# Performance work log

Measured on AMD Instinct MI355X. Metric: run time of the kernel, lower is better.

The kernel has to match this reference:

```python
import jax, jax.numpy as jnp
import numpy as np

N = 30000          # nodes
E = 480000         # edges (before self-loops)
G = 64             # graphs in batch
EMB = 64
IN = 6 + 2 * EMB   # 134
H1, C1 = 4, 128    # gat1 heads / out channels
H2, C2 = 1, 256    # gat2
LRELU_SLOPE = 0.2


def _layernorm(x, g, b, eps=1e-5):
    m = x.mean(-1, keepdims=True)
    v = ((x - m) ** 2).mean(-1, keepdims=True)
    return (x - m) / jnp.sqrt(v + eps) * g + b


def _gatv2(x, src, dst, Wl, bl, Wr, br, att, bias, H, C, n, concat):
    # GATv2 (PyG semantics, share_weights=False, eval mode -> no dropout)
    xl = (x @ Wl + bl).reshape(n, H, C)   # source transform
    xr = (x @ Wr + br).reshape(n, H, C)   # target transform
    # e_ij = att . leaky_relu(xl_j + xr_i), edges j->i : [E_tot, H]
    e = jnp.sum(jax.nn.leaky_relu(xl[src] + xr[dst], LRELU_SLOPE) * att, axis=-1)
    # scatter-softmax over incoming edges of each target node
    emax = jax.lax.stop_gradient(jax.ops.segment_max(e, dst, num_segments=n))
    ex = jnp.exp(e - emax[dst])
    den = jax.ops.segment_sum(ex, dst, num_segments=n)
    alpha = ex / (den[dst] + 1e-16)                       # [E_tot, H]
    out = jax.ops.segment_sum(alpha[:, :, None] * xl[src], dst, num_segments=n)
    if concat:
        return out.reshape(n, H * C) + bias
    return out.mean(axis=1) + bias


def setup_inputs() -> dict:
    key = jax.random.key(0)
    ks = jax.random.split(key, 24)
    s = 0.05
    inp = {
        "x_cont": jax.random.normal(ks[0], (N, 6), jnp.float32),
        "x_class": jax.random.randint(ks[1], (N,), 0, 12, jnp.int32),
        "x_pitch": jax.random.randint(ks[2], (N,), 0, 129, jnp.int32),
        "edge_index": jax.random.randint(ks[3], (2, E), 0, N, jnp.int32),
        "batch": jnp.sort(jax.random.randint(ks[4], (N,), 0, G, jnp.int32)),
        "class_tab": jax.random.normal(ks[5], (12, EMB), jnp.float32) * s,
        "pitch_tab": jax.random.normal(ks[6], (129, EMB), jnp.float32) * s,
        "Wl1": jax.random.normal(ks[7], (IN, H1 * C1), jnp.float32) * s,
        "bl1": jnp.zeros((H1 * C1,), jnp.float32),
        "Wr1": jax.random.normal(ks[8], (IN, H1 * C1), jnp.float32) * s,
        "br1": jnp.zeros((H1 * C1,), jnp.float32),
        "att1": jax.random.normal(ks[9], (H1, C1), jnp.float32) * s,
        "bias1": jnp.zeros((H1 * C1,), jnp.float32),
        "ln1_g": jnp.ones((H1 * C1,), jnp.float32),
        "ln1_b": jnp.zeros((H1 * C1,), jnp.float32),
        "Wl2": jax.random.normal(ks[10], (H1 * C1, H2 * C2), jnp.float32) * s,
        "bl2": jnp.zeros((H2 * C2,), jnp.float32),
        "Wr2": jax.random.normal(ks[11], (H1 * C1, H2 * C2), jnp.float32) * s,
        "br2": jnp.zeros((H2 * C2,), jnp.float32),
        "att2": jax.random.normal(ks[12], (H2, C2), jnp.float32) * s,
        "bias2": jnp.zeros((C2,), jnp.float32),
        "ln2_g": jnp.ones((C2,), jnp.float32),
        "ln2_b": jnp.zeros((C2,), jnp.float32),
        "Wp1": jax.random.normal(ks[13], (C2, 512), jnp.float32) * s,
        "bp1": jnp.zeros((512,), jnp.float32),
        "lnp_g": jnp.ones((512,), jnp.float32),
        "lnp_b": jnp.zeros((512,), jnp.float32),
        "Wp2": jax.random.normal(ks[14], (512, 512), jnp.float32) * s,
        "bp2": jnp.zeros((512,), jnp.float32),
    }
    return inp


def reference(x_cont, x_class, x_pitch, edge_index, batch,
              class_tab, pitch_tab,
              Wl1, bl1, Wr1, br1, att1, bias1, ln1_g, ln1_b,
              Wl2, bl2, Wr2, br2, att2, bias2, ln2_g, ln2_b,
              Wp1, bp1, lnp_g, lnp_b, Wp2, bp2):
    # node features: [N, 6 + 64 + 64]
    x = jnp.concatenate([x_cont, class_tab[x_class], pitch_tab[x_pitch]], axis=1)
    # add self-loops (PyG GATv2Conv default)
    loops = jnp.arange(N, dtype=edge_index.dtype)
    src = jnp.concatenate([edge_index[0], loops])
    dst = jnp.concatenate([edge_index[1], loops])
    x = jax.nn.elu(_layernorm(_gatv2(x, src, dst, Wl1, bl1, Wr1, br1, att1, bias1, H1, C1, N, True), ln1_g, ln1_b))
    x = jax.nn.elu(_layernorm(_gatv2(x, src, dst, Wl2, bl2, Wr2, br2, att2, bias2, H2, C2, N, False), ln2_g, ln2_b))
    # global mean pool over graphs
    sums = jax.ops.segment_sum(x, batch, num_segments=G)
    cnt = jax.ops.segment_sum(jnp.ones((N,), x.dtype), batch, num_segments=G)
    pooled = sums / jnp.maximum(cnt, 1.0)[:, None]
    # projection head + L2 normalize
    h = jax.nn.gelu(_layernorm(pooled @ Wp1 + bp1, lnp_g, lnp_b), approximate=False)
    out = h @ Wp2 + bp2
    norm = jnp.sqrt(jnp.sum(out * out, axis=1, keepdims=True))
    return out / jnp.maximum(norm, 1e-12)
```

## Files before the change

kernel.cpp:

```cpp
#include <hip/hip_runtime.h>
#include <math.h>

#define NG 64

typedef short bf16x8 __attribute__((ext_vector_type(8)));
typedef short bf16x4 __attribute__((ext_vector_type(4)));
typedef float f32x4 __attribute__((ext_vector_type(4)));

#define LOG2E 1.4426950408889634f

static inline int cdiv(int a, int b) { return (a + b - 1) / b; }

__device__ inline ushort f2b(float f) {
  union { float f; uint u; } v; v.f = f;
  uint u = v.u;
  return (ushort)((u + 0x7fffu + ((u >> 16) & 1u)) >> 16);
}

__device__ __forceinline__ void unpack8(bf16x8 vb, float* v) {
  union { bf16x8 b; uint u[4]; } cv; cv.b = vb;
#pragma unroll
  for (int q = 0; q < 4; ++q) {
    union { uint u; float f; } lo, hi;
    lo.u = cv.u[q] << 16;
    hi.u = cv.u[q] & 0xffff0000u;
    v[2 * q] = lo.f; v[2 * q + 1] = hi.f;
  }
}
__device__ __forceinline__ void unpack4(bf16x4 vb, float* v) {
  union { bf16x4 b; uint u[2]; } cv; cv.b = vb;
#pragma unroll
  for (int q = 0; q < 2; ++q) {
    union { uint u; float f; } lo, hi;
    lo.u = cv.u[q] << 16;
    hi.u = cv.u[q] & 0xffff0000u;
    v[2 * q] = lo.f; v[2 * q + 1] = hi.f;
  }
}

__device__ __forceinline__ float dppsum16(float x) {
  union { float f; int i; } a, b;
  a.f = x;
  b.i = __builtin_amdgcn_update_dpp(0, a.i, 0x121, 0xF, 0xF, true); a.f += b.f;
  b.i = __builtin_amdgcn_update_dpp(0, a.i, 0x122, 0xF, 0xF, true); a.f += b.f;
  b.i = __builtin_amdgcn_update_dpp(0, a.i, 0x124, 0xF, 0xF, true); a.f += b.f;
  b.i = __builtin_amdgcn_update_dpp(0, a.i, 0x128, 0xF, 0xF, true); a.f += b.f;
  return a.f;
}

// ... 89 lines not shown
}

__global__ __launch_bounds__(256) void k_scatter(
    const int* __restrict__ src, const int* __restrict__ dst,
    const int* __restrict__ rowptr, int* __restrict__ fill,
    int* __restrict__ csr, int E, int N) {
  int t = blockIdx.x * blockDim.x + threadIdx.x;
  int s, d;
  if (t < E) { s = src[t]; d = dst[t]; }
  else if (t < E + N) { s = t - E; d = t - E; }
  else if (t < E + N + 8) { csr[t] = 0; return; }
  else return;
  int pos = rowptr[d] + atomicAdd(&fill[d], 1);
  csr[pos] = s;
}

#define GBM 128
#define GBN 128
#define GBK 32
#define ESTRIDE 136
__device__ __forceinline__ int swzf(int r, int s) {
  return r * 64 + ((s * 16) ^ (((r >> 1) & 3) << 4));
}
__global__ __launch_bounds__(256) void k_gemm_mfma(
    const ushort* __restrict__ A, const ushort* __restrict__ Bt,
    const float* __restrict__ blo, const float* __restrict__ bhi, int nhalf,
    ushort* __restrict__ Clo, ushort* __restrict__ Chi, int M, int Kp) {
  __shared__ ushort smem[GBM * ESTRIDE];
  ushort* sA = smem;
  ushort* sB = smem + GBM * GBK;
  int tid = threadIdx.x;
  int lane = tid & 63, w = tid >> 6;
  int wr = w >> 1, wc = w & 1;
  int row0 = blockIdx.x * GBM, col0 = blockIdx.y * GBN;
  int nK = Kp / GBK;

  int rs = tid >> 2, ss = tid & 3;
  int wO0 = swzf(rs, ss);
  int wO1 = swzf(rs + 64, ss);
  bool okA0 = (row0 + rs) < M;
  bool okA1 = (row0 + rs + 64) < M;
  size_t baseA0 = (size_t)(row0 + rs) * Kp + ss * 8;
  size_t baseA1 = (size_t)(row0 + rs + 64) * Kp + ss * 8;
  size_t baseB0 = (size_t)(col0 + rs) * Kp + ss * 8;
  size_t baseB1 = (size_t)(col0 + rs + 64) * Kp + ss * 8;

  int fr = lane & 15, kq = lane >> 4;
  int aoff[4], boff[4];
#pragma unroll
  for (int m = 0; m < 4; ++m) {
    int ra = wr * 64 + m * 16 + fr;
    aoff[m] = ra * 64 + ((kq * 16) ^ (((ra >> 1) & 3) << 4));
    int rb = wc * 64 + m * 16 + fr;
    boff[m] = rb * 64 + ((kq * 16) ^ (((rb >> 1) & 3) << 4));
  }

  f32x4 acc[4][4] = {};
  bf16x8 zz = {};
  bf16x8 pa0, pa1, pb0, pb1, qa0, qa1, qb0, qb1;

#define LOADG(KS, RA0, RA1, RB0, RB1)                                   \
  do {                                                                  \
    const ushort* ap = A + (size_t)(KS) * GBK;                          \
    const ushort* bp = Bt + (size_t)(KS) * GBK;                         \
    RA0 = okA0 ? *(const bf16x8*)(ap + baseA0) : zz;                    \
    RA1 = okA1 ? *(const bf16x8*)(ap + baseA1) : zz;                    \
    RB0 = *(const bf16x8*)(bp + baseB0);                                \
// ... 37 lines not shown

  __syncthreads();
#pragma unroll
  for (int m = 0; m < 4; ++m) {
#pragma unroll
    for (int n = 0; n < 4; ++n) {
      int tc = wc * 64 + n * 16 + fr;
      float bv = ((col0 + tc) < nhalf) ? blo[col0 + tc] : bhi[col0 + tc - nhalf];
#pragma unroll
      for (int j = 0; j < 4; ++j) {
        int tr = wr * 64 + m * 16 + kq * 4 + j;
        smem[tr * ESTRIDE + tc] = f2b(acc[m][n][j] + bv);
      }
    }
  }
  __syncthreads();
  ushort* Cd = (col0 < nhalf) ? Clo : Chi;
  int cb0 = (col0 < nhalf) ? col0 : col0 - nhalf;
  int r0 = tid >> 4, cb = (tid & 15) * 8;
#pragma unroll
  for (int pass = 0; pass < 8; ++pass) {
    int r = pass * 16 + r0;
    int grow = row0 + r;
    if (grow < M) {
      bf16x8 vv = *(const bf16x8*)&smem[r * ESTRIDE + cb];
      *(bf16x8*)&Cd[(size_t)grow * nhalf + cb0 + cb] = vv;
    }
  }
#undef LOADG
#undef STAGE
#undef COMPUTE
}

__global__ __launch_bounds__(256, 4) void k_gat1(
    const ushort* __restrict__ xl, const ushort* __restrict__ xr,
    const int* __restrict__ rowptr, const int* __restrict__ csr,
    const float* __restrict__ att, const float* __restrict__ bias,
    const float* __restrict__ lng, const float* __restrict__ lnb,
    ushort* __restrict__ out, int n) {
  int lane = threadIdx.x & 63;
  int wid = __builtin_amdgcn_readfirstlane((int)((blockIdx.x * blockDim.x + threadIdx.x) >> 6));
  if (wid >= n) return;
  int base = lane * 8;
  float xrv[8], a6[8], a4[8];
  {
    bf16x8 t = *(const bf16x8*)(xr + (size_t)wid * 512 + base);
    unpack8(t, xrv);
#pragma unroll
    for (int j = 0; j < 8; ++j) {
      float a = att[base + j] * LOG2E;
      a6[j] = 0.6f * a;
      a4[j] = 0.4f * a;
    }
  }
  float s = 0.f;
  float acc[8] = {};
  int e0 = rowptr[wid], e1 = rowptr[wid + 1];
  int last = e1 - 1;

#define LROW1(ROW) (*(const bf16x8*)(xl + (size_t)(ROW) * 512 + base))
  bf16x8 r0 = LROW1(csr[e0]);
  bf16x8 r1 = LROW1(csr[min(e0 + 1, last)]);
  bf16x8 r2 = LROW1(csr[min(e0 + 2, last)]);
  bf16x8 r3 = LROW1(csr[min(e0 + 3, last)]);

  for (int pp = e0; pp < e1; pp += 4) {
    int i0 = csr[min(pp + 4, last)], i1 = csr[min(pp + 5, last)];
    int i2 = csr[min(pp + 6, last)], i3 = csr[min(pp + 7, last)];
    bf16x8 c0 = r0, c1 = r1, c2 = r2, c3 = r3;
    r0 = LROW1(i0); r1 = LROW1(i1); r2 = LROW1(i2); r3 = LROW1(i3);
    float v0[8], v1[8], v2[8], v3[8];
    unpack8(c0, v0); unpack8(c1, v1); unpack8(c2, v2); unpack8(c3, v3);
    float p0 = 0.f, p1 = 0.f, p2 = 0.f, p3 = 0.f;
#pragma unroll
    for (int j = 0; j < 8; ++j) {
      float t0 = v0[j] + xrv[j];
      float t1 = v1[j] + xrv[j];
      float t2 = v2[j] + xrv[j];
      float t3 = v3[j] + xrv[j];
      p0 = fmaf(a6[j], t0, fmaf(a4[j], fabsf(t0), p0));
      p1 = fmaf(a6[j], t1, fmaf(a4[j], fabsf(t1), p1));
      p2 = fmaf(a6[j], t2, fmaf(a4[j], fabsf(t2), p2));
      p3 = fmaf(a6[j], t3, fmaf(a4[j], fabsf(t3), p3));
    }
    float pe0 = dppsum16(p0);
    float pe1 = dppsum16(p1);
    float pe2 = dppsum16(p2);
    float pe3 = dppsum16(p3);
    float w0 = exp2f(pe0 - 8.f * LOG2E);
    float w1 = (pp + 1 <= last) ? exp2f(pe1 - 8.f * LOG2E) : 0.f;
    float w2 = (pp + 2 <= last) ? exp2f(pe2 - 8.f * LOG2E) : 0.f;
    float w3 = (pp + 3 <= last) ? exp2f(pe3 - 8.f * LOG2E) : 0.f;
    s += (w0 + w1) + (w2 + w3);
#pragma unroll
    for (int j = 0; j < 8; ++j) {
      float t = fmaf(w0, v0[j], acc[j]);
      t = fmaf(w1, v1[j], t);
      t = fmaf(w2, v2[j], t);
      acc[j] = fmaf(w3, v3[j], t);
    }
  }
#undef LROW1
  float inv = 1.f / s;
  float o[8];
#pragma unroll
  for (int j = 0; j < 8; ++j) o[j] = acc[j] * inv + bias[base + j];
  float sum = 0.f, sq = 0.f;
#pragma unroll
  for (int j = 0; j < 8; ++j) { sum += o[j]; sq += o[j] * o[j]; }
  sum = dppsum16(sum); sq = dppsum16(sq);
  sum += __shfl_xor(sum, 16); sq += __shfl_xor(sq, 16);
  sum += __shfl_xor(sum, 32); sq += __shfl_xor(sq, 32);
  float mean = sum * (1.f / 512.f);
  float var = fmaxf(sq * (1.f / 512.f) - mean * mean, 0.f);
  float rstd = rsqrtf(var + 1e-5f);
  bf16x8 ov;
#pragma unroll
  for (int j = 0; j < 8; ++j) {
    float y = (o[j] - mean) * rstd * lng[base + j] + lnb[base + j];
    y = y > 0.f ? y : __expf(y) - 1.f;
    ov[j] = (short)f2b(y);
  }
  *(bf16x8*)&out[(size_t)wid * 512 + base] = ov;
}

__global__ __launch_bounds__(256, 4) void k_gat2(
    const ushort* __restrict__ xl, const ushort* __restrict__ xr,
    const int* __restrict__ rowptr, const int* __restrict__ csr,
    const float* __restrict__ att, const float* __restrict__ bias,
    const float* __restrict__ lng, const float* __restrict__ lnb,
    float* __restrict__ out, int n) {
  int lane = threadIdx.x & 63;
  int wid = __builtin_amdgcn_readfirstlane((int)((blockIdx.x * blockDim.x + threadIdx.x) >> 6));
  if (wid >= n) return;
  int base = lane * 4;
  float xrv[4], a6[4], a4[4];
  {
    bf16x4 t = *(const bf16x4*)(xr + (size_t)wid * 256 + base);
    unpack4(t, xrv);
#pragma unroll
    for (int j = 0; j < 4; ++j) {
      float a = att[base + j] * LOG2E;
      a6[j] = 0.6f * a;
      a4[j] = 0.4f * a;
    }
  }
  float s = 0.f;
  float acc[4] = {};
  int e0 = rowptr[wid], e1 = rowptr[wid + 1];
  int last = e1 - 1;

#define LROW2(ROW) (*(const bf16x4*)(xl + (size_t)(ROW) * 256 + base))
  bf16x4 r0 = LROW2(csr[e0]);
  bf16x4 r1 = LROW2(csr[min(e0 + 1, last)]);
  bf16x4 r2 = LROW2(csr[min(e0 + 2, last)]);
  bf16x4 r3 = LROW2(csr[min(e0 + 3, last)]);

  for (int pp = e0; pp < e1; pp += 4) {
    int i0 = csr[min(pp + 4, last)], i1 = csr[min(pp + 5, last)];
    int i2 = csr[min(pp + 6, last)], i3 = csr[min(pp + 7, last)];
    bf16x4 c0 = r0, c1 = r1, c2 = r2, c3 = r3;
    r0 = LROW2(i0); r1 = LROW2(i1); r2 = LROW2(i2); r3 = LROW2(i3);
    float v0[4], v1[4], v2[4], v3[4];
    unpack4(c0, v0); unpack4(c1, v1); unpack4(c2, v2); unpack4(c3, v3);
    float p0 = 0.f, p1 = 0.f, p2 = 0.f, p3 = 0.f;
#pragma unroll
    for (int j = 0; j < 4; ++j) {
      float t0 = v0[j] + xrv[j];
      float t1 = v1[j] + xrv[j];
      float t2 = v2[j] + xrv[j];
      float t3 = v3[j] + xrv[j];
      p0 = fmaf(a6[j], t0, fmaf(a4[j], fabsf(t0), p0));
      p1 = fmaf(a6[j], t1, fmaf(a4[j], fabsf(t1), p1));
      p2 = fmaf(a6[j], t2, fmaf(a4[j], fabsf(t2), p2));
      p3 = fmaf(a6[j], t3, fmaf(a4[j], fabsf(t3), p3));
    }
    float pe0 = dppsum16(p0);
    float pe1 = dppsum16(p1);
    float pe2 = dppsum16(p2);
    float pe3 = dppsum16(p3);
    pe0 += __shfl_xor(pe0, 16); pe1 += __shfl_xor(pe1, 16);
    pe2 += __shfl_xor(pe2, 16); pe3 += __shfl_xor(pe3, 16);
    pe0 += __shfl_xor(pe0, 32); pe1 += __shfl_xor(pe1, 32);
    pe2 += __shfl_xor(pe2, 32); pe3 += __shfl_xor(pe3, 32);
    float w0 = exp2f(pe0 - 8.f * LOG2E);
    float w1 = (pp + 1 <= last) ? exp2f(pe1 - 8.f * LOG2E) : 0.f;
    float w2 = (pp + 2 <= last) ? exp2f(pe2 - 8.f * LOG2E) : 0.f;
    float w3 = (pp + 3 <= last) ? exp2f(pe3 - 8.f * LOG2E) : 0.f;
    s += (w0 + w1) + (w2 + w3);
#pragma unroll
    for (int j = 0; j < 4; ++j) {
      float t = fmaf(w0, v0[j], acc[j]);
      t = fmaf(w1, v1[j], t);
      t = fmaf(w2, v2[j], t);
      acc[j] = fmaf(w3, v3[j], t);
    }
  }
#undef LROW2
  float inv = 1.f / s;
  float o[4];
#pragma unroll
  for (int j = 0; j < 4; ++j) o[j] = acc[j] * inv + bias[base + j];
  float sum = 0.f, sq = 0.f;
#pragma unroll
  for (int j = 0; j < 4; ++j) { sum += o[j]; sq += o[j] * o[j]; }
  sum = dppsum16(sum); sq = dppsum16(sq);
  sum += __shfl_xor(sum, 16); sq += __shfl_xor(sq, 16);
  sum += __shfl_xor(sum, 32); sq += __shfl_xor(sq, 32);
  float mean = sum * (1.f / 256.f);
  float var = fmaxf(sq * (1.f / 256.f) - mean * mean, 0.f);
  float rstd = rsqrtf(var + 1e-5f);
#pragma unroll
  for (int j = 0; j < 4; ++j) {
    float y = (o[j] - mean) * rstd * lng[base + j] + lnb[base + j];
    y = y > 0.f ? y : __expf(y) - 1.f;
    out[(size_t)wid * 256 + base + j] = y;
  }
}

__global__ __launch_bounds__(256) void k_pool(
    const float* __restrict__ h2, const int* __restrict__ batch,
    float* __restrict__ pooled, int* __restrict__ cnt, int n) {
  int c = threadIdx.x;
  int n0 = blockIdx.x * 64;
  int n1 = min(n0 + 64, n);
  if (n0 >= n) return;
  float acc = 0.f;
  int cur = batch[n0];
  int cl = 0;
  for (int i = n0; i < n1; ++i) {
    int bb = batch[i];
    if (bb != cur) {
      atomicAdd(&pooled[cur * 256 + c], acc);
      if (c == 0) atomicAdd(&cnt[cur], cl);
      acc = 0.f; cl = 0; cur = bb;
    }
    acc += h2[(size_t)i * 256 + c];
    cl++;
  }
  atomicAdd(&pooled[cur * 256 + c], acc);
  if (c == 0) atomicAdd(&cnt[cur], cl);
}

__global__ __launch_bounds__(512) void k_proj1(
    const float* __restrict__ pooled, const int* __restrict__ cnt,
    const float* __restrict__ W, const float* __restrict__ b,
    const float* __restrict__ lng, const float* __restrict__ lnb,
    float* __restrict__ hout) {
  __shared__ float row[256];
  __shared__ float red[16];
  int g = blockIdx.x, c = threadIdx.x;
  if (c < 256) {
    float cc = fmaxf((float)cnt[g], 1.f);
    row[c] = pooled[g * 256 + c] / cc;
  }
  __syncthreads();
  float acc = b[c];
#pragma unroll 4
  for (int k = 0; k < 256; ++k) acc += row[k] * W[k * 512 + c];
  float sum = acc, sq = acc * acc;
#pragma unroll
  for (int off = 1; off < 64; off <<= 1) {
    sum += __shfl_xor(sum, off);
    sq += __shfl_xor(sq, off);
  }
  int wv = threadIdx.x >> 6;
  if ((threadIdx.x & 63) == 0) { red[wv] = sum; red[8 + wv] = sq; }
  __syncthreads();
  float S = 0.f, Q = 0.f;
#pragma unroll
// ... 58 lines not shown
  const float* ln2b = (const float*)d_in[22];
  const float* Wp1 = (const float*)d_in[23];
  const float* bp1 = (const float*)d_in[24];
  const float* lnpg = (const float*)d_in[25];
  const float* lnpb = (const float*)d_in[26];
  const float* Wp2 = (const float*)d_in[27];
  const float* bp2 = (const float*)d_in[28];
  float* out = (float*)d_out;
  (void)n_in; (void)out_size; (void)ws_size;

  int N = in_sizes[1];
  int E = in_sizes[3] / 2;
  int ET = E + N;
  int NB = cdiv(N, 256);

  char* p = (char*)d_ws;
  ushort* xb   = (ushort*)p; p += (size_t)N * 160 * 2;
  ushort* W1t  = (ushort*)p; p += (size_t)1024 * 160 * 2;
  ushort* W2t  = (ushort*)p; p += (size_t)512 * 512 * 2;
  ushort* xl1  = (ushort*)p; p += (size_t)N * 512 * 2;
  ushort* xr1  = (ushort*)p; p += (size_t)N * 512 * 2;
  ushort* h1b  = (ushort*)p; p += (size_t)N * 512 * 2;
  float* pooled = (float*)p; p += (size_t)NG * 256 * 4;
  int* cnt     = (int*)p;    p += NG * 4;
  float* hproj = (float*)p;  p += (size_t)NG * 512 * 4;
  int* deg     = (int*)p;    p += (size_t)N * 4;
  int* fill    = (int*)p;    p += (size_t)N * 4;
  int* rowptr  = (int*)p;    p += (size_t)(N + 1) * 4;
  int* csr     = (int*)p;    p += (size_t)(ET + 8) * 4;
  int* bsum    = (int*)p;    p += 256 * 4;
  int* boff    = (int*)p;    p += 256 * 4;
  ushort* xl2 = xl1;
  ushort* xr2 = xl1 + (size_t)N * 256;
  float* h2   = (float*)xr1;

  const int* esrc = ei;
  const int* edst = ei + E;

  hipMemsetAsync(deg, 0, (size_t)2 * N * sizeof(int), stream);
  hipMemsetAsync(pooled, 0, (size_t)NG * 256 * sizeof(float) + NG * sizeof(int), stream);

  int prep_total = N * 160 + 1024 * 160 + 512 * 512 + ET;
  k_prep<<<cdiv(prep_total, 256), 256, 0, stream>>>(
      x_cont, x_class, x_pitch, ctab, ptab, Wl1, Wr1, Wl2, Wr2, edst,
      xb, W1t, W2t, deg, N, E);
  k_bsum<<<NB, 256, 0, stream>>>(deg, bsum, N);
  k_scanb<<<1, 256, 0, stream>>>(bsum, boff, NB);
  k_scanc<<<NB, 256, 0, stream>>>(deg, boff, rowptr, N);
  k_scatter<<<cdiv(ET + 8, 256), 256, 0, stream>>>(esrc, edst, rowptr, fill, csr, E, N);

  dim3 g1(cdiv(N, GBM), 1024 / GBN);
  k_gemm_mfma<<<g1, 256, 0, stream>>>(xb, W1t, bl1, br1, 512, xl1, xr1, N, 160);
  k_gat1<<<cdiv(N * 64, 256), 256, 0, stream>>>(xl1, xr1, rowptr, csr, att1, bias1, ln1g, ln1b, h1b, N);

  dim3 g2(cdiv(N, GBM), 512 / GBN);
  k_gemm_mfma<<<g2, 256, 0, stream>>>(h1b, W2t, bl2, br2, 256, xl2, xr2, N, 512);
  k_gat2<<<cdiv(N * 64, 256), 256, 0, stream>>>(xl2, xr2, rowptr, csr, att2, bias2, ln2g, ln2b, h2, N);

  k_pool<<<cdiv(N, 64), 256, 0, stream>>>(h2, batch, pooled, cnt, N);
  k_proj1<<<NG, 512, 0, stream>>>(pooled, cnt, Wp1, bp1, lnpg, lnpb, hproj);
  k_proj2<<<NG, 512, 0, stream>>>(hproj, Wp2, bp2, out);
}
```

Baseline: 333.7 us.

## Enlarge GAT blocks, split score accumulators, store layer-2 output as bf16

Both GAT aggregation kernels now launch 1024-thread blocks with launch bounds (1024, 8), which pushes for more resident waves to hide gather latency at the cost of register pressure. The attention-score dot products use two interleaved accumulators per edge to shorten FMA dependency chains. The layer-2 output is written as bf16 instead of fp32 and converted back in the pooling kernel, halving that write and read traffic while adding rounding error before pooling.

After: 497.2 us. +49.0%, slower.

```diff
diff --git a/kernel.cpp b/kernel.cpp
--- a/kernel.cpp
+++ b/kernel.cpp
@@ -15,6 +15,10 @@
   union { float f; uint u; } v; v.f = f;
   uint u = v.u;
   return (ushort)((u + 0x7fffu + ((u >> 16) & 1u)) >> 16);
+}
+__device__ inline float b2f(ushort h) {
+  union { uint u; float f; } v; v.u = ((uint)h) << 16;
+  return v.f;
 }
 
 __device__ __forceinline__ void unpack8(bf16x8 vb, float* v) {
@@ -274,7 +278,7 @@
 #undef COMPUTE
 }
 
-__global__ __launch_bounds__(256, 4) void k_gat1(
+__global__ __launch_bounds__(1024, 8) void k_gat1(
     const ushort* __restrict__ xl, const ushort* __restrict__ xr,
     const int* __restrict__ rowptr, const int* __restrict__ csr,
     const float* __restrict__ att, const float* __restrict__ bias,
@@ -313,22 +317,28 @@
     r0 = LROW1(i0); r1 = LROW1(i1); r2 = LROW1(i2); r3 = LROW1(i3);
     float v0[8], v1[8], v2[8], v3[8];
     unpack8(c0, v0); unpack8(c1, v1); unpack8(c2, v2); unpack8(c3, v3);
-    float p0 = 0.f, p1 = 0.f, p2 = 0.f, p3 = 0.f;
-#pragma unroll
-    for (int j = 0; j < 8; ++j) {
-      float t0 = v0[j] + xrv[j];
-      float t1 = v1[j] + xrv[j];
-      float t2 = v2[j] + xrv[j];
-      float t3 = v3[j] + xrv[j];
-      p0 = fmaf(a6[j], t0, fmaf(a4[j], fabsf(t0), p0));
-      p1 = fmaf(a6[j], t1, fmaf(a4[j], fabsf(t1), p1));
-      p2 = fmaf(a6[j], t2, fmaf(a4[j], fabsf(t2), p2));
-      p3 = fmaf(a6[j], t3, fmaf(a4[j], fabsf(t3), p3));
-    }
-    float pe0 = dppsum16(p0);
-    float pe1 = dppsum16(p1);
-    float pe2 = dppsum16(p2);
-    float pe3 = dppsum16(p3);
+    float p0a = 0.f, p0b = 0.f, p1a = 0.f, p1b = 0.f;
+    float p2a = 0.f, p2b = 0.f, p3a = 0.f, p3b = 0.f;
+#pragma unroll
+    for (int q = 0; q < 4; ++q) {
+      int ja = 2 * q, jb = 2 * q + 1;
+      float t0a = v0[ja] + xrv[ja], t0b = v0[jb] + xrv[jb];
+      float t1a = v1[ja] + xrv[ja], t1b = v1[jb] + xrv[jb];
+      float t2a = v2[ja] + xrv[ja], t2b = v2[jb] + xrv[jb];
+      float t3a = v3[ja] + xrv[ja], t3b = v3[jb] + xrv[jb];
+      p0a = fmaf(a6[ja], t0a, fmaf(a4[ja], fabsf(t0a), p0a));
+      p0b = fmaf(a6[jb], t0b, fmaf(a4[jb], fabsf(t0b), p0b));
+      p1a = fmaf(a6[ja], t1a, fmaf(a4[ja], fabsf(t1a), p1a));
+      p1b = fmaf(a6[jb], t1b, fmaf(a4[jb], fabsf(t1b), p1b));
+      p2a = fmaf(a6[ja], t2a, fmaf(a4[ja], fabsf(t2a), p2a));
+      p2b = fmaf(a6[jb], t2b, fmaf(a4[jb], fabsf(t2b), p2b));
+      p3a = fmaf(a6[ja], t3a, fmaf(a4[ja], fabsf(t3a), p3a));
+      p3b = fmaf(a6[jb], t3b, fmaf(a4[jb], fabsf(t3b), p3b));
+    }
+    float pe0 = dppsum16(p0a + p0b);
+    float pe1 = dppsum16(p1a + p1b);
+    float pe2 = dppsum16(p2a + p2b);
+    float pe3 = dppsum16(p3a + p3b);
     float w0 = exp2f(pe0 - 8.f * LOG2E);
     float w1 = (pp + 1 <= last) ? exp2f(pe1 - 8.f * LOG2E) : 0.f;
     float w2 = (pp + 2 <= last) ? exp2f(pe2 - 8.f * LOG2E) : 0.f;
@@ -366,12 +376,12 @@
   *(bf16x8*)&out[(size_t)wid * 512 + base] = ov;
 }
 
-__global__ __launch_bounds__(256, 4) void k_gat2(
+__global__ __launch_bounds__(1024, 8) void k_gat2(
     const ushort* __restrict__ xl, const ushort* __restrict__ xr,
     const int* __restrict__ rowptr, const int* __restrict__ csr,
     const float* __restrict__ att, const float* __restrict__ bias,
     const float* __restrict__ lng, const float* __restrict__ lnb,
-    float* __restrict__ out, int n) {
+    ushort* __restrict__ out, int n) {
   int lane = threadIdx.x & 63;
   int wid = __builtin_amdgcn_readfirstlane((int)((blockIdx.x * blockDim.x + threadIdx.x) >> 6));
   if (wid >= n) return;
@@ -405,22 +415,28 @@
     r0 = LROW2(i0); r1 = LROW2(i1); r2 = LROW2(i2); r3 = LROW2(i3);
     float v0[4], v1[4], v2[4], v3[4];
     unpack4(c0, v0); unpack4(c1, v1); unpack4(c2, v2); unpack4(c3, v3);
-    float p0 = 0.f, p1 = 0.f, p2 = 0.f, p3 = 0.f;
-#pragma unroll
-    for (int j = 0; j < 4; ++j) {
-      float t0 = v0[j] + xrv[j];
-      float t1 = v1[j] + xrv[j];
-      float t2 = v2[j] + xrv[j];
-      float t3 = v3[j] + xrv[j];
-      p0 = fmaf(a6[j], t0, fmaf(a4[j], fabsf(t0), p0));
-      p1 = fmaf(a6[j], t1, fmaf(a4[j], fabsf(t1), p1));
-      p2 = fmaf(a6[j], t2, fmaf(a4[j], fabsf(t2), p2));
-      p3 = fmaf(a6[j], t3, fmaf(a4[j], fabsf(t3), p3));
-    }
-    float pe0 = dppsum16(p0);
-    float pe1 = dppsum16(p1);
-    float pe2 = dppsum16(p2);
-    float pe3 = dppsum16(p3);
+    float p0a = 0.f, p0b = 0.f, p1a = 0.f, p1b = 0.f;
+    float p2a = 0.f, p2b = 0.f, p3a = 0.f, p3b = 0.f;
+#pragma unroll
+    for (int q = 0; q < 2; ++q) {
+      int ja = 2 * q, jb = 2 * q + 1;
+      float t0a = v0[ja] + xrv[ja], t0b = v0[jb] + xrv[jb];
+      float t1a = v1[ja] + xrv[ja], t1b = v1[jb] + xrv[jb];
+      float t2a = v2[ja] + xrv[ja], t2b = v2[jb] + xrv[jb];
+      float t3a = v3[ja] + xrv[ja], t3b = v3[jb] + xrv[jb];
+      p0a = fmaf(a6[ja], t0a, fmaf(a4[ja], fabsf(t0a), p0a));
+      p0b = fmaf(a6[jb], t0b, fmaf(a4[jb], fabsf(t0b), p0b));
+      p1a = fmaf(a6[ja], t1a, fmaf(a4[ja], fabsf(t1a), p1a));
+      p1b = fmaf(a6[jb], t1b, fmaf(a4[jb], fabsf(t1b), p1b));
+      p2a = fmaf(a6[ja], t2a, fmaf(a4[ja], fabsf(t2a), p2a));
+      p2b = fmaf(a6[jb], t2b, fmaf(a4[jb], fabsf(t2b), p2b));
+      p3a = fmaf(a6[ja], t3a, fmaf(a4[ja], fabsf(t3a), p3a));
+      p3b = fmaf(a6[jb], t3b, fmaf(a4[jb], fabsf(t3b), p3b));
+    }
+    float pe0 = dppsum16(p0a + p0b);
+    float pe1 = dppsum16(p1a + p1b);
+    float pe2 = dppsum16(p2a + p2b);
+    float pe3 = dppsum16(p3a + p3b);
     pe0 += __shfl_xor(pe0, 16); pe1 += __shfl_xor(pe1, 16);
     pe2 += __shfl_xor(pe2, 16); pe3 += __shfl_xor(pe3, 16);
     pe0 += __shfl_xor(pe0, 32); pe1 += __shfl_xor(pe1, 32);
@@ -452,16 +468,18 @@
   float mean = sum * (1.f / 256.f);
   float var = fmaxf(sq * (1.f / 256.f) - mean * mean, 0.f);
   float rstd = rsqrtf(var + 1e-5f);
+  bf16x4 ov;
 #pragma unroll
   for (int j = 0; j < 4; ++j) {
     float y = (o[j] - mean) * rstd * lng[base + j] + lnb[base + j];
     y = y > 0.f ? y : __expf(y) - 1.f;
-    out[(size_t)wid * 256 + base + j] = y;
-  }
+    ov[j] = (short)f2b(y);
+  }
+  *(bf16x4*)&out[(size_t)wid * 256 + base] = ov;
 }
 
 __global__ __launch_bounds__(256) void k_pool(
-    const float* __restrict__ h2, const int* __restrict__ batch,
+    const ushort* __restrict__ h2, const int* __restrict__ batch,
     float* __restrict__ pooled, int* __restrict__ cnt, int n) {
   int c = threadIdx.x;
   int n0 = blockIdx.x * 64;
@@ -477,7 +495,7 @@
       if (c == 0) atomicAdd(&cnt[cur], cl);
       acc = 0.f; cl = 0; cur = bb;
     }
-    acc += h2[(size_t)i * 256 + c];
+    acc += b2f(h2[(size_t)i * 256 + c]);
     cl++;
   }
   atomicAdd(&pooled[cur * 256 + c], acc);
@@ -602,7 +620,7 @@
   int* boff    = (int*)p;    p += 256 * 4;
   ushort* xl2 = xl1;
   ushort* xr2 = xl1 + (size_t)N * 256;
-  float* h2   = (float*)xr1;
+  ushort* h2  = xr1;
 
   const int* esrc = ei;
   const int* edst = ei + E;
@@ -621,11 +639,11 @@
 
   dim3 g1(cdiv(N, GBM), 1024 / GBN);
   k_gemm_mfma<<<g1, 256, 0, stream>>>(xb, W1t, bl1, br1, 512, xl1, xr1, N, 160);
-  k_gat1<<<cdiv(N * 64, 256), 256, 0, stream>>>(xl1, xr1, rowptr, csr, att1, bias1, ln1g, ln1b, h1b, N);
+  k_gat1<<<cdiv(N * 64, 1024), 1024, 0, stream>>>(xl1, xr1, rowptr, csr, att1, bias1, ln1g, ln1b, h1b, N);
 
   dim3 g2(cdiv(N, GBM), 512 / GBN);
   k_gemm_mfma<<<g2, 256, 0, stream>>>(h1b, W2t, bl2, br2, 256, xl2, xr2, N, 512);
-  k_gat2<<<cdiv(N * 64, 256), 256, 0, stream>>>(xl2, xr2, rowptr, csr, att2, bias2, ln2g, ln2b, h2, N);
+  k_gat2<<<cdiv(N * 64, 1024), 1024, 0, stream>>>(xl2, xr2, rowptr, csr, att2, bias2, ln2g, ln2b, h2, N);
 
   k_pool<<<cdiv(N, 64), 256, 0, stream>>>(h2, batch, pooled, cnt, N);
   k_proj1<<<NG, 512, 0, stream>>>(pooled, cnt, Wp1, bp1, lnpg, lnpb, hproj);
```

## Process two nodes per wavefront in GAT kernels, bf16 h2, swap GEMM grid order

Applied to the files above, without the earlier changes.

Each wavefront in the GAT aggregation kernels now handles two target nodes at once and interleaves their neighbor gathers, so more independent loads are in flight. The dot-product reduction is split into two partial sums to shorten the dependency chain. The layer-2 output is stored as bf16 instead of fp32, which halves the bytes the pool kernel reads, at some precision cost. The GEMM grid swaps its x/y axes so column tiles of the same row block run next to each other for better A-tile cache reuse. Pairing nodes of different degrees wastes work up to the larger degree and adds register pressure (launch bounds lowered to 3).

Result: slower. 351.0 us (+5.2%).

```diff
diff --git a/kernel.cpp b/kernel.cpp
--- a/kernel.cpp
+++ b/kernel.cpp
@@ -15,6 +15,10 @@
   union { float f; uint u; } v; v.f = f;
   uint u = v.u;
   return (ushort)((u + 0x7fffu + ((u >> 16) & 1u)) >> 16);
+}
+__device__ inline float b2f(ushort h) {
+  union { uint u; float f; } v; v.u = ((uint)h) << 16;
+  return v.f;
 }
 
 __device__ __forceinline__ void unpack8(bf16x8 vb, float* v) {
@@ -170,7 +174,7 @@
   int tid = threadIdx.x;
   int lane = tid & 63, w = tid >> 6;
   int wr = w >> 1, wc = w & 1;
-  int row0 = blockIdx.x * GBM, col0 = blockIdx.y * GBN;
+  int row0 = blockIdx.y * GBM, col0 = blockIdx.x * GBN;
   int nK = Kp / GBK;
 
   int rs = tid >> 2, ss = tid & 3;
@@ -274,194 +278,262 @@
 #undef COMPUTE
 }
 
-__global__ __launch_bounds__(256, 4) void k_gat1(
+__global__ __launch_bounds__(256, 3) void k_gat1(
     const ushort* __restrict__ xl, const ushort* __restrict__ xr,
     const int* __restrict__ rowptr, const int* __restrict__ csr,
     const float* __restrict__ att, const float* __restrict__ bias,
     const float* __restrict__ lng, const float* __restrict__ lnb,
     ushort* __restrict__ out, int n) {
   int lane = threadIdx.x & 63;
-  int wid = __builtin_amdgcn_readfirstlane((int)((blockIdx.x * blockDim.x + threadIdx.x) >> 6));
-  if (wid >= n) return;
+  int wp = __builtin_amdgcn_readfirstlane((int)((blockIdx.x * blockDim.x + threadIdx.x) >> 6));
+  int widA = wp * 2;
+  if (widA >= n) return;
+  bool hasB = (widA + 1) < n;
+  int widB = hasB ? widA + 1 : widA;
   int base = lane * 8;
-  float xrv[8], a6[8], a4[8];
-  {
-    bf16x8 t = *(const bf16x8*)(xr + (size_t)wid * 512 + base);
-    unpack8(t, xrv);
-#pragma unroll
-    for (int j = 0; j < 8; ++j) {
-      float a = att[base + j] * LOG2E;
-      a6[j] = 0.6f * a;
-      a4[j] = 0.4f * a;
-    }
-  }
-  float s = 0.f;
-  float acc[8] = {};
-  int e0 = rowptr[wid], e1 = rowptr[wid + 1];
-  int last = e1 - 1;
+  float a6[8], a4[8];
+#pragma unroll
+  for (int j = 0; j < 8; ++j) {
+    float a = att[base + j] * LOG2E;
+    a6[j] = 0.6f * a;
+    a4[j] = 0.4f * a;
+  }
+  float xrA[8], xrB[8];
+  unpack8(*(const bf16x8*)(xr + (size_t)widA * 512 + base), xrA);
+  unpack8(*(const bf16x8*)(xr + (size_t)widB * 512 + base), xrB);
+  float sA = 0.f, sB = 0.f;
+  float accA[8] = {}, accB[8] = {};
+  int eA0 = rowptr[widA], dA = rowptr[widA + 1] - eA0, lastA = eA0 + dA - 1;
+  int eB0 = rowptr[widB], dB = rowptr[widB + 1] - eB0, lastB = eB0 + dB - 1;
+  int dmax = max(dA, dB);
 
 #define LROW1(ROW) (*(const bf16x8*)(xl + (size_t)(ROW) * 512 + base))
-  bf16x8 r0 = LROW1(csr[e0]);
-  bf16x8 r1 = LROW1(csr[min(e0 + 1, last)]);
-  bf16x8 r2 = LROW1(csr[min(e0 + 2, last)]);
-  bf16x8 r3 = LROW1(csr[min(e0 + 3, last)]);
-
-  for (int pp = e0; pp < e1; pp += 4) {
-    int i0 = csr[min(pp + 4, last)], i1 = csr[min(pp + 5, last)];
-    int i2 = csr[min(pp + 6, last)], i3 = csr[min(pp + 7, last)];
-    bf16x8 c0 = r0, c1 = r1, c2 = r2, c3 = r3;
-    r0 = LROW1(i0); r1 = LROW1(i1); r2 = LROW1(i2); r3 = LROW1(i3);
-    float v0[8], v1[8], v2[8], v3[8];
-    unpack8(c0, v0); unpack8(c1, v1); unpack8(c2, v2); unpack8(c3, v3);
-    float p0 = 0.f, p1 = 0.f, p2 = 0.f, p3 = 0.f;
-#pragma unroll
-    for (int j = 0; j < 8; ++j) {
-      float t0 = v0[j] + xrv[j];
-      float t1 = v1[j] + xrv[j];
-      float t2 = v2[j] + xrv[j];
-      float t3 = v3[j] + xrv[j];
-      p0 = fmaf(a6[j], t0, fmaf(a4[j], fabsf(t0), p0));
-      p1 = fmaf(a6[j], t1, fmaf(a4[j], fabsf(t1), p1));
-      p2 = fmaf(a6[j], t2, fmaf(a4[j], fabsf(t2), p2));
-      p3 = fmaf(a6[j], t3, fmaf(a4[j], fabsf(t3), p3));
-    }
-    float pe0 = dppsum16(p0);
-    float pe1 = dppsum16(p1);
-    float pe2 = dppsum16(p2);
-    float pe3 = dppsum16(p3);
-    float w0 = exp2f(pe0 - 8.f * LOG2E);
-    float w1 = (pp + 1 <= last) ? exp2f(pe1 - 8.f * LOG2E) : 0.f;
-    float w2 = (pp + 2 <= last) ? exp2f(pe2 - 8.f * LOG2E) : 0.f;
-    float w3 = (pp + 3 <= last) ? exp2f(pe3 - 8.f * LOG2E) : 0.f;
-    s += (w0 + w1) + (w2 + w3);
-#pragma unroll
-    for (int j = 0; j < 8; ++j) {
-      float t = fmaf(w0, v0[j], acc[j]);
-      t = fmaf(w1, v1[j], t);
-      t = fmaf(w2, v2[j], t);
-      acc[j] = fmaf(w3, v3[j], t);
-    }
-  }
+  bf16x8 ra0 = LROW1(csr[eA0]);
+  bf16x8 ra1 = LROW1(csr[min(eA0 + 1, lastA)]);
+  bf16x8 ra2 = LROW1(csr[min(eA0 + 2, lastA)]);
+  bf16x8 ra3 = LROW1(csr[min(eA0 + 3, lastA)]);
+  bf16x8 rb0 = LROW1(csr[eB0]);
+  bf16x8 rb1 = LROW1(csr[min(eB0 + 1, lastB)]);
+  bf16x8 rb2 = LROW1(csr[min(eB0 + 2, lastB)]);
+  bf16x8 rb3 = LROW1(csr[min(eB0 + 3, lastB)]);
+
+#define GSTEP1(C0, C1, C2, C3, XRV, SS, ACC, P0, LASTV)                        \
+  do {                                                                         \
+    float v0[8], v1[8], v2[8], v3[8];                                          \
+    unpack8(C0, v0); unpack8(C1, v1); unpack8(C2, v2); unpack8(C3, v3);        \
+    float p0a = 0.f, p0b = 0.f, p1a = 0.f, p1b = 0.f;                          \
+    float p2a = 0.f, p2b = 0.f, p3a = 0.f, p3b = 0.f;                          \
+    _Pragma("unroll") for (int q = 0; q < 4; ++q) {                            \
+      int ja = 2 * q, jb = 2 * q + 1;                                          \
+      float t0a = v0[ja] + XRV[ja], t0b = v0[jb] + XRV[jb];                    \
+      float t1a = v1[ja] + XRV[ja], t1b = v1[jb] + XRV[jb];                    \
+      float t2a = v2[ja] + XRV[ja], t2b = v2[jb] + XRV[jb];                    \
+      float t3a = v3[ja] + XRV[ja], t3b = v3[jb] + XRV[jb];                    \
+      p0a = fmaf(a6[ja], t0a, fmaf(a4[ja], fabsf(t0a), p0a));                  \
+      p0b = fmaf(a6[jb], t0b, fmaf(a4[jb], fabsf(t0b), p0b));                  \
+      p1a = fmaf(a6[ja], t1a, fmaf(a4[ja], fabsf(t1a), p1a));                  \
+      p1b = fmaf(a6[jb], t1b, fmaf(a4[jb], fabsf(t1b), p1b));                  \
+      p2a = fmaf(a6[ja], t2a, fmaf(a4[ja], fabsf(t2a), p2a));                  \
+      p2b = fmaf(a6[jb], t2b, fmaf(a4[jb], fabsf(t2b), p2b));                  \
+      p3a = fmaf(a6[ja], t3a, fmaf(a4[ja], fabsf(t3a), p3a));                  \
+      p3b = fmaf(a6[jb], t3b, fmaf(a4[jb], fabsf(t3b), p3b));                  \
+    }                                                                          \
+    float pe0 = dppsum16(p0a + p0b);                                           \
+    float pe1 = dppsum16(p1a + p1b);                                           \
+    float pe2 = dppsum16(p2a + p2b);                                           \
+    float pe3 = dppsum16(p3a + p3b);                                           \
+    float w0 = ((P0) <= (LASTV)) ? exp2f(pe0 - 8.f * LOG2E) : 0.f;             \
+    float w1 = ((P0) + 1 <= (LASTV)) ? exp2f(pe1 - 8.f * LOG2E) : 0.f;         \
+    float w2 = ((P0) + 2 <= (LASTV)) ? exp2f(pe2 - 8.f * LOG2E) : 0.f;         \
+    float w3 = ((P0) + 3 <= (LASTV)) ? exp2f(pe3 - 8.f * LOG2E) : 0.f;         \
+    SS += (w0 + w1) + (w2 + w3);                                               \
+    _Pragma("unroll") for (int j = 0; j < 8; ++j) {                            \
+      float t = fmaf(w0, v0[j], ACC[j]);                                       \
+      t = fmaf(w1, v1[j], t);                                                  \
+      t = fmaf(w2, v2[j], t);                                                  \
+      ACC[j] = fmaf(w3, v3[j], t);                                             \
+    }                                                                          \
+  } while (0)
+
+  for (int it = 0; it < dmax; it += 4) {
+    int pA = eA0 + it, pB = eB0 + it;
+    bf16x8 cA0 = ra0, cA1 = ra1, cA2 = ra2, cA3 = ra3;
+    bf16x8 cB0 = rb0, cB1 = rb1, cB2 = rb2, cB3 = rb3;
+    ra0 = LROW1(csr[min(pA + 4, lastA)]);
+    ra1 = LROW1(csr[min(pA + 5, lastA)]);
+    ra2 = LROW1(csr[min(pA + 6, lastA)]);
+    ra3 = LROW1(csr[min(pA + 7, lastA)]);
+    rb0 = LROW1(csr[min(pB + 4, lastB)]);
+    rb1 = LROW1(csr[min(pB + 5, lastB)]);
+    rb2 = LROW1(csr[min(pB + 6, lastB)]);
+    rb3 = LROW1(csr[min(pB + 7, lastB)]);
+    GSTEP1(cA0, cA1, cA2, cA3, xrA, sA, accA, pA, lastA);
+    GSTEP1(cB0, cB1, cB2, cB3, xrB, sB, accB, pB, lastB);
+  }
+#undef GSTEP1
 #undef LROW1
-  float inv = 1.f / s;
-  float o[8];
-#pragma unroll
-  for (int j = 0; j < 8; ++j) o[j] = acc[j] * inv + bias[base + j];
-  float sum = 0.f, sq = 0.f;
-#pragma unroll
-  for (int j = 0; j < 8; ++j) { sum += o[j]; sq += o[j] * o[j]; }
-  sum = dppsum16(sum); sq = dppsum16(sq);
-  sum += __shfl_xor(sum, 16); sq += __shfl_xor(sq, 16);
-  sum += __shfl_xor(sum, 32); sq += __shfl_xor(sq, 32);
-  float mean = sum * (1.f / 512.f);
-  float var = fmaxf(sq * (1.f / 512.f) - mean * mean, 0.f);
-  float rstd = rsqrtf(var + 1e-5f);
-  bf16x8 ov;
-#pragma unroll
-  for (int j = 0; j < 8; ++j) {
-    float y = (o[j] - mean) * rstd * lng[base + j] + lnb[base + j];
-    y = y > 0.f ? y : __expf(y) - 1.f;
-    ov[j] = (short)f2b(y);
-  }
-  *(bf16x8*)&out[(size_t)wid * 512 + base] = ov;
-}
-
-__global__ __launch_bounds__(256, 4) void k_gat2(
+
+#define EPI1(SS, ACC, WID)                                                     \
+  do {                                                                         \
+    float inv = 1.f / SS;                                                      \
+    float o[8];                                                                \
+    _Pragma("unroll") for (int j = 0; j < 8; ++j)                              \
+        o[j] = ACC[j] * inv + bias[base + j];                                  \
+    float sum = 0.f, sq = 0.f;                                                 \
+    _Pragma("unroll") for (int j = 0; j < 8; ++j) {                            \
+      sum += o[j]; sq += o[j] * o[j];                                          \
+    }                                                                          \
+    sum = dppsum16(sum); sq = dppsum16(sq);                                    \
+    sum += __shfl_xor(sum, 16); sq += __shfl_xor(sq, 16);                      \
+    sum += __shfl_xor(sum, 32); sq += __shfl_xor(sq, 32);                      \
+    float mean = sum * (1.f / 512.f);                                          \
+    float var = fmaxf(sq * (1.f / 512.f) - mean * mean, 0.f);                  \
+    float rstd = rsqrtf(var + 1e-5f);                                          \
+    bf16x8 ov;                                                                 \
+    _Pragma("unroll") for (int j = 0; j < 8; ++j) {                            \
+      float y = (o[j] - mean) * rstd * lng[base + j] + lnb[base + j];          \
+      y = y > 0.f ? y : __expf(y) - 1.f;                                       \
+      ov[j] = (short)f2b(y);                                                   \
+    }                                                                          \
+    *(bf16x8*)&out[(size_t)(WID) * 512 + base] = ov;                           \
+  } while (0)
+
+  EPI1(sA, accA, widA);
+  if (hasB) EPI1(sB, accB, widB);
+#undef EPI1
+}
+
+__global__ __launch_bounds__(256, 3) void k_gat2(
     const ushort* __restrict__ xl, const ushort* __restrict__ xr,
     const int* __restrict__ rowptr, const int* __restrict__ csr,
     const float* __restrict__ att, const float* __restrict__ bias,
     const float* __restrict__ lng, const float* __restrict__ lnb,
-    float* __restrict__ out, int n) {
+    ushort* __restrict__ out, int n) {
   int lane = threadIdx.x & 63;
-  int wid = __builtin_amdgcn_readfirstlane((int)((blockIdx.x * blockDim.x + threadIdx.x) >> 6));
-  if (wid >= n) return;
+  int wp = __builtin_amdgcn_readfirstlane((int)((blockIdx.x * blockDim.x + threadIdx.x) >> 6));
+  int widA = wp * 2;
+  if (widA >= n) return;
+  bool hasB = (widA + 1) < n;
+  int widB = hasB ? widA + 1 : widA;
   int base = lane * 4;
-  float xrv[4], a6[4], a4[4];
-  {
-    bf16x4 t = *(const bf16x4*)(xr + (size_t)wid * 256 + base);
-    unpack4(t, xrv);
-#pragma unroll
-    for (int j = 0; j < 4; ++j) {
-      float a = att[base + j] * LOG2E;
-      a6[j] = 0.6f * a;
-      a4[j] = 0.4f * a;
-    }
-  }
-  float s = 0.f;
-  float acc[4] = {};
-  int e0 = rowptr[wid], e1 = rowptr[wid + 1];
-  int last = e1 - 1;
+  float a6[4], a4[4];
+#pragma unroll
+  for (int j = 0; j < 4; ++j) {
+    float a = att[base + j] * LOG2E;
+    a6[j] = 0.6f * a;
+    a4[j] = 0.4f * a;
+  }
+  float xrA[4], xrB[4];
+  unpack4(*(const bf16x4*)(xr + (size_t)widA * 256 + base), xrA);
+  unpack4(*(const bf16x4*)(xr + (size_t)widB * 256 + base), xrB);
+  float sA = 0.f, sB = 0.f;
+  float accA[4] = {}, accB[4] = {};
+  int eA0 = rowptr[widA], dA = rowptr[widA + 1] - eA0, lastA = eA0 + dA - 1;
+  int eB0 = rowptr[widB], dB = rowptr[widB + 1] - eB0, lastB = eB0 + dB - 1;
+  int dmax = max(dA, dB);
 
 #define LROW2(ROW) (*(const bf16x4*)(xl + (size_t)(ROW) * 256 + base))
-  bf16x4 r0 = LROW2(csr[e0]);
-  bf16x4 r1 = LROW2(csr[min(e0 + 1, last)]);
-  bf16x4 r2 = LROW2(csr[min(e0 + 2, last)]);
-  bf16x4 r3 = LROW2(csr[min(e0 + 3, last)]);
-
-  for (int pp = e0; pp < e1; pp += 4) {
-    int i0 = csr[min(pp + 4, last)], i1 = csr[min(pp + 5, last)];
-    int i2 = csr[min(pp + 6, last)], i3 = csr[min(pp + 7, last)];
-    bf16x4 c0 = r0, c1 = r1, c2 = r2, c3 = r3;
-    r0 = LROW2(i0); r1 = LROW2(i1); r2 = LROW2(i2); r3 = LROW2(i3);
-    float v0[4], v1[4], v2[4], v3[4];
-    unpack4(c0, v0); unpack4(c1, v1); unpack4(c2, v2); unpack4(c3, v3);
-    float p0 = 0.f, p1 = 0.f, p2 = 0.f, p3 = 0.f;
-#pragma unroll
-    for (int j = 0; j < 4; ++j) {
-      float t0 = v0[j] + xrv[j];
-      float t1 = v1[j] + xrv[j];
-      float t2 = v2[j] + xrv[j];
-      float t3 = v3[j] + xrv[j];
-      p0 = fmaf(a6[j], t0, fmaf(a4[j], fabsf(t0), p0));
-      p1 = fmaf(a6[j], t1, fmaf(a4[j], fabsf(t1), p1));
-      p2 = fmaf(a6[j], t2, fmaf(a4[j], fabsf(t2), p2));
-      p3 = fmaf(a6[j], t3, fmaf(a4[j], fabsf(t3), p3));
-    }
-    float pe0 = dppsum16(p0);
-    float pe1 = dppsum16(p1);
-    float pe2 = dppsum16(p2);
-    float pe3 = dppsum16(p3);
-    pe0 += __shfl_xor(pe0, 16); pe1 += __shfl_xor(pe1, 16);
-    pe2 += __shfl_xor(pe2, 16); pe3 += __shfl_xor(pe3, 16);
-    pe0 += __shfl_xor(pe0, 32); pe1 += __shfl_xor(pe1, 32);
-    pe2 += __shfl_xor(pe2, 32); pe3 += __shfl_xor(pe3, 32);
-    float w0 = exp2f(pe0 - 8.f * LOG2E);
-    float w1 = (pp + 1 <= last) ? exp2f(pe1 - 8.f * LOG2E) : 0.f;
-    float w2 = (pp + 2 <= last) ? exp2f(pe2 - 8.f * LOG2E) : 0.f;
-    float w3 = (pp + 3 <= last) ? exp2f(pe3 - 8.f * LOG2E) : 0.f;
-    s += (w0 + w1) + (w2 + w3);
-#pragma unroll
-    for (int j = 0; j < 4; ++j) {
-      float t = fmaf(w0, v0[j], acc[j]);
-      t = fmaf(w1, v1[j], t);
-      t = fmaf(w2, v2[j], t);
-      acc[j] = fmaf(w3, v3[j], t);
-    }
-  }
+  bf16x4 ra0 = LROW2(csr[eA0]);
+  bf16x4 ra1 = LROW2(csr[min(eA0 + 1, lastA)]);
+  bf16x4 ra2 = LROW2(csr[min(eA0 + 2, lastA)]);
+  bf16x4 ra3 = LROW2(csr[min(eA0 + 3, lastA)]);
+  bf16x4 rb0 = LROW2(csr[eB0]);
+  bf16x4 rb1 = LROW2(csr[min(eB0 + 1, lastB)]);
+  bf16x4 rb2 = LROW2(csr[min(eB0 + 2, lastB)]);
+  bf16x4 rb3 = LROW2(csr[min(eB0 + 3, lastB)]);
+
+#define GSTEP2(C0, C1, C2, C3, XRV, SS, ACC, P0, LASTV)                        \
+  do {                                                                         \
+    float v0[4], v1[4], v2[4], v3[4];                                          \
+    unpack4(C0, v0); unpack4(C1, v1); unpack4(C2, v2); unpack4(C3, v3);        \
+    float p0a = 0.f, p0b = 0.f, p1a = 0.f, p1b = 0.f;                          \
+    float p2a = 0.f, p2b = 0.f, p3a = 0.f, p3b = 0.f;                          \
+    _Pragma("unroll") for (int q = 0; q < 2; ++q) {                            \
+      int ja = 2 * q, jb = 2 * q + 1;                                          \
+      float t0a = v0[ja] + XRV[ja], t0b = v0[jb] + XRV[jb];                    \
+      float t1a = v1[ja] + XRV[ja], t1b = v1[jb] + XRV[jb];                    \
+      float t2a = v2[ja] + XRV[ja], t2b = v2[jb] + XRV[jb];                    \
+      float t3a = v3[ja] + XRV[ja], t3b = v3[jb] + XRV[jb];                    \
+      p0a = fmaf(a6[ja], t0a, fmaf(a4[ja], fabsf(t0a), p0a));                  \
+      p0b = fmaf(a6[jb], t0b, fmaf(a4[jb], fabsf(t0b), p0b));                  \
+      p1a = fmaf(a6[ja], t1a, fmaf(a4[ja], fabsf(t1a), p1a));                  \
+      p1b = fmaf(a6[jb], t1b, fmaf(a4[jb], fabsf(t1b), p1b));                  \
+      p2a = fmaf(a6[ja], t2a, fmaf(a4[ja], fabsf(t2a), p2a));                  \
+      p2b = fmaf(a6[jb], t2b, fmaf(a4[jb], fabsf(t2b), p2b));                  \
+      p3a = fmaf(a6[ja], t3a, fmaf(a4[ja], fabsf(t3a), p3a));                  \
+      p3b = fmaf(a6[jb], t3b, fmaf(a4[jb], fabsf(t3b), p3b));                  \
+    }                                                                          \
+    float pe0 = dppsum16(p0a + p0b);                                           \
+    float pe1 = dppsum16(p1a + p1b);                                           \
+    float pe2 = dppsum16(p2a + p2b);                                           \
+    float pe3 = dppsum16(p3a + p3b);                                           \
+    pe0 += __shfl_xor(pe0, 16); pe1 += __shfl_xor(pe1, 16);                    \
+    pe2 += __shfl_xor(pe2, 16); pe3 += __shfl_xor(pe3, 16);                    \
+    pe0 += __shfl_xor(pe0, 32); pe1 += __shfl_xor(pe1, 32);                    \
+    pe2 += __shfl_xor(pe2, 32); pe3 += __shfl_xor(pe3, 32);                    \
+    float w0 = ((P0) <= (LASTV)) ? exp2f(pe0 - 8.f * LOG2E) : 0.f;             \
+    float w1 = ((P0) + 1 <= (LASTV)) ? exp2f(pe1 - 8.f * LOG2E) : 0.f;         \
+    float w2 = ((P0) + 2 <= (LASTV)) ? exp2f(pe2 - 8.f * LOG2E) : 0.f;         \
+    float w3 = ((P0) + 3 <= (LASTV)) ? exp2f(pe3 - 8.f * LOG2E) : 0.f;         \
+    SS += (w0 + w1) + (w2 + w3);                                               \
+    _Pragma("unroll") for (int j = 0; j < 4; ++j) {                            \
+      float t = fmaf(w0, v0[j], ACC[j]);                                       \
+      t = fmaf(w1, v1[j], t);                                                  \
+      t = fmaf(w2, v2[j], t);                                                  \
+      ACC[j] = fmaf(w3, v3[j], t);                                             \
+    }                                                                          \
+  } while (0)
+
+  for (int it = 0; it < dmax; it += 4) {
+    int pA = eA0 + it, pB = eB0 + it;
+    bf16x4 cA0 = ra0, cA1 = ra1, cA2 = ra2, cA3 = ra3;
+    bf16x4 cB0 = rb0, cB1 = rb1, cB2 = rb2, cB3 = rb3;
+    ra0 = LROW2(csr[min(pA + 4, lastA)]);
+    ra1 = LROW2(csr[min(pA + 5, lastA)]);
+    ra2 = LROW2(csr[min(pA + 6, lastA)]);
+    ra3 = LROW2(csr[min(pA + 7, lastA)]);
+    rb0 = LROW2(csr[min(pB + 4, lastB)]);
+    rb1 = LROW2(csr[min(pB + 5, lastB)]);
+    rb2 = LROW2(csr[min(pB + 6, lastB)]);
+    rb3 = LROW2(csr[min(pB + 7, lastB)]);
+    GSTEP2(cA0, cA1, cA2, cA3, xrA, sA, accA, pA, lastA);
+    GSTEP2(cB0, cB1, cB2, cB3, xrB, sB, accB, pB, lastB);
+  }
+#undef GSTEP2
 #undef LROW2
-  float inv = 1.f / s;
-  float o[4];
-#pragma unroll
-  for (int j = 0; j < 4; ++j) o[j] = acc[j] * inv + bias[base + j];
-  float sum = 0.f, sq = 0.f;
-#pragma unroll
-  for (int j = 0; j < 4; ++j) { sum += o[j]; sq += o[j] * o[j]; }
-  sum = dppsum16(sum); sq = dppsum16(sq);
-  sum += __shfl_xor(sum, 16); sq += __shfl_xor(sq, 16);
-  sum += __shfl_xor(sum, 32); sq += __shfl_xor(sq, 32);
-  float mean = sum * (1.f / 256.f);
-  float var = fmaxf(sq * (1.f / 256.f) - mean * mean, 0.f);
-  float rstd = rsqrtf(var + 1e-5f);
-#pragma unroll
-  for (int j = 0; j < 4; ++j) {
-    float y = (o[j] - mean) * rstd * lng[base + j] + lnb[base + j];
-    y = y > 0.f ? y : __expf(y) - 1.f;
-    out[(size_t)wid * 256 + base + j] = y;
-  }
+
+#define EPI2(SS, ACC, WID)                                                     \
+  do {                                                                         \
+    float inv = 1.f / SS;                                                      \
+    float o[4];                                                                \
+    _Pragma("unroll") for (int j = 0; j < 4; ++j)                              \
+        o[j] = ACC[j] * inv + bias[base + j];                                  \
+    float sum = 0.f, sq = 0.f;                                                 \
+    _Pragma("unroll") for (int j = 0; j < 4; ++j) {                            \
+      sum += o[j]; sq += o[j] * o[j];                                          \
+    }                                                                          \
+    sum = dppsum16(sum); sq = dppsum16(sq);                                    \
+    sum += __shfl_xor(sum, 16); sq += __shfl_xor(sq, 16);                      \
+    sum += __shfl_xor(sum, 32); sq += __shfl_xor(sq, 32);                      \
+    float mean = sum * (1.f / 256.f);                                          \
+    float var = fmaxf(sq * (1.f / 256.f) - mean * mean, 0.f);                  \
+    float rstd = rsqrtf(var + 1e-5f);                                          \
+    bf16x4 ov;                                                                 \
+    _Pragma("unroll") for (int j = 0; j < 4; ++j) {                            \
+      float y = (o[j] - mean) * rstd * lng[base + j] + lnb[base + j];          \
+      y = y > 0.f ? y : __expf(y) - 1.f;                                       \
+      ov[j] = (short)f2b(y);                                                   \
+    }                                                                          \
+    *(bf16x4*)&out[(size_t)(WID) * 256 + base] = ov;                           \
+  } while (0)
+
+  EPI2(sA, accA, widA);
+  if (hasB) EPI2(sB, accB, widB);
+#undef EPI2
 }
 
 __global__ __launch_bounds__(256) void k_pool(
-    const float* __restrict__ h2, const int* __restrict__ batch,
+    const ushort* __restrict__ h2, const int* __restrict__ batch,
     float* __restrict__ pooled, int* __restrict__ cnt, int n) {
   int c = threadIdx.x;
   int n0 = blockIdx.x * 64;
@@ -477,7 +549,7 @@
       if (c == 0) atomicAdd(&cnt[cur], cl);
       acc = 0.f; cl = 0; cur = bb;
     }
-    acc += h2[(size_t)i * 256 + c];
+    acc += b2f(h2[(size_t)i * 256 + c]);
     cl++;
   }
   atomicAdd(&pooled[cur * 256 + c], acc);
@@ -602,7 +674,7 @@
   int* boff    = (int*)p;    p += 256 * 4;
   ushort* xl2 = xl1;
   ushort* xr2 = xl1 + (size_t)N * 256;
-  float* h2   = (float*)xr1;
+  ushort* h2  = xr1;
 
   const int* esrc = ei;
   const int* edst = ei + E;
@@ -619,13 +691,13 @@
   k_scanc<<<NB, 256, 0, stream>>>(deg, boff, rowptr, N);
   k_scatter<<<cdiv(ET + 8, 256), 256, 0, stream>>>(esrc, edst, rowptr, fill, csr, E, N);
 
-  dim3 g1(cdiv(N, GBM), 1024 / GBN);
+  dim3 g1(1024 / GBN, cdiv(N, GBM));
   k_gemm_mfma<<<g1, 256, 0, stream>>>(xb, W1t, bl1, br1, 512, xl1, xr1, N, 160);
-  k_gat1<<<cdiv(N * 64, 256), 256, 0, stream>>>(xl1, xr1, rowptr, csr, att1, bias1, ln1g, ln1b, h1b, N);
-
-  dim3 g2(cdiv(N, GBM), 512 / GBN);
+  k_gat1<<<cdiv(N, 8), 256, 0, stream>>>(xl1, xr1, rowptr, csr, att1, bias1, ln1g, ln1b, h1b, N);
+
+  dim3 g2(512 / GBN, cdiv(N, GBM));
   k_gemm_mfma<<<g2, 256, 0, stream>>>(h1b, W2t, bl2, br2, 256, xl2, xr2, N, 512);
-  k_gat2<<<cdiv(N * 64, 256), 256, 0, stream>>>(xl2, xr2, rowptr, csr, att2, bias2, ln2g, ln2b, h2, N);
+  k_gat2<<<cdiv(N, 8), 256, 0, stream>>>(xl2, xr2, rowptr, csr, att2, bias2, ln2g, ln2b, h2, N);
 
   k_pool<<<cdiv(N, 64), 256, 0, stream>>>(h2, batch, pooled, cnt, N);
   k_proj1<<<NG, 512, 0, stream>>>(pooled, cnt, Wp1, bp1, lnpg, lnpb, hproj);
```
